# Kernel optimization log

Hardware: AMD Instinct MI355X
Metric: run time of the kernel (lower is better)

## Reference

```python
import jax, jax.numpy as jnp
import numpy as np

DIM = 1024
HEADS = 16
HEAD_DIM = DIM // HEADS


def setup_inputs() -> dict:
    key = jax.random.key(0)
    k_x, k_qkv, k_ow, k_ob = jax.random.split(key, 4)
    x = jax.random.normal(k_x, (2, 2048, DIM), dtype=jnp.float32)
    # nn.Linear(dim, 3*dim, bias=False): weight shape [3*dim, dim], y = x @ W.T
    w_qkv = jax.random.normal(k_qkv, (3 * DIM, DIM), dtype=jnp.float32) * (DIM ** -0.5)
    # nn.Linear(dim, dim) with bias
    w_o = jax.random.normal(k_ow, (DIM, DIM), dtype=jnp.float32) * (DIM ** -0.5)
    b_o = jax.random.normal(k_ob, (DIM,), dtype=jnp.float32) * 0.02
    return {"x": x, "w_qkv": w_qkv, "w_o": w_o, "b_o": b_o}


def reference(x, w_qkv, w_o, b_o):
    b, n, _ = x.shape
    scale = DIM ** -0.5  # NOTE: source scales by full dim, not head dim
    # qkv projection: [b, n, 3*dim]
    qkv = jnp.einsum('bnd,ed->bne', x, w_qkv)
    # 'b n (qkv h d) -> qkv b h n d'
    qkv = qkv.reshape(b, n, 3, HEADS, HEAD_DIM)
    q = jnp.transpose(qkv[:, :, 0], (0, 2, 1, 3))  # [b, h, n, d]
    k = jnp.transpose(qkv[:, :, 1], (0, 2, 1, 3))
    v = jnp.transpose(qkv[:, :, 2], (0, 2, 1, 3))
    scores = jnp.einsum('bhqd,bhkd->bhqk', q, k) * scale  # [b, h, n, n]
    attn = jax.nn.softmax(scores, axis=-1)
    out = jnp.einsum('bhqk,bhkd->bhqd', attn, v)  # [b, h, n, d]
    out = jnp.transpose(out, (0, 2, 1, 3)).reshape(b, n, DIM)  # 'b h n d -> b n (h d)'
    out = jnp.einsum('bnd,ed->bne', out, w_o) + b_o
    return out
```

## Files before the change

### kernel.cpp

```cpp
#include <hip/hip_runtime.h>
#include <stdint.h>


#define DIM 1024
#define SEQ 2048
#define BATCH 2
#define ROWS 4096
#define RSTRIDE 3072

typedef __bf16 bf16_t;
typedef bf16_t bf16x4 __attribute__((ext_vector_type(4)));
typedef bf16_t bf16x8 __attribute__((ext_vector_type(8)));
typedef float f32x4 __attribute__((ext_vector_type(4)));

__device__ __forceinline__ ushort f2bf(float f) {
    uint32_t u;
    __builtin_memcpy(&u, &f, 4);
    uint32_t r = (u + 0x7fffu + ((u >> 16) & 1u)) >> 16;
    return (ushort)r;
}

__device__ __forceinline__ void store_out(ushort* p, float v) { *p = f2bf(v); }
__device__ __forceinline__ void store_out(float* p, float v) { *p = v; }

__device__ __forceinline__ void gl_lds16(const void* g, void* l) {
    __builtin_amdgcn_global_load_lds(
        (const __attribute__((address_space(1))) void*)g,
        (__attribute__((address_space(3))) void*)l, 16, 0, 0);
}

__global__ __launch_bounds__(256) void cvt_kernel(
    const float* __restrict__ src, ushort* __restrict__ dst) {
    int i = (blockIdx.x * 256 + threadIdx.x) * 8;
    float4 a = *(const float4*)(src + i);
    float4 b = *(const float4*)(src + i + 4);
    uint4 u;
    u.x = (uint)f2bf(a.x) | ((uint)f2bf(a.y) << 16);
    u.y = (uint)f2bf(a.z) | ((uint)f2bf(a.w) << 16);
    u.z = (uint)f2bf(b.x) | ((uint)f2bf(b.y) << 16);
    u.w = (uint)f2bf(b.z) | ((uint)f2bf(b.w) << 16);
    *(uint4*)(dst + i) = u;
}

template <typename OutT>
__global__ __launch_bounds__(256) void gemm_bt_kernel(
    const ushort* __restrict__ A, const ushort* __restrict__ B,
    const float* __restrict__ bias, OutT* __restrict__ C,
    int M, int N, int K) {
    __shared__ __align__(16) ushort sA[128 * 64];
    __shared__ __align__(16) ushort sB[128 * 64];

    const int tid = threadIdx.x;
    const int lane = tid & 63, w = tid >> 6;
    const int quad = lane >> 4, l15 = lane & 15;
    const int wm = (w >> 1) * 64, wn = (w & 1) * 64;
    const int bm = blockIdx.y, bn = blockIdx.x;

    f32x4 acc[4][4];
#pragma unroll
    for (int i = 0; i < 4; i++)
#pragma unroll
        for (int j = 0; j < 4; j++) acc[i][j] = (f32x4){0.f, 0.f, 0.f, 0.f};

    const ushort* Abase = A + (size_t)(bm * 128) * K;
    const ushort* Bbase = B + (size_t)(bn * 128) * K;
    const int rd = lane >> 3, c8 = lane & 7;
    const int sw = l15 & 7;

    for (int kk = 0; kk < K; kk += 64) {
        __syncthreads();
#pragma unroll
        for (int t = 0; t < 4; t++) {
            int row = w * 32 + t * 8;
            gl_lds16(Abase + (size_t)(row + rd) * K + kk + ((c8 ^ rd) * 8),
                     sA + row * 64);
            gl_lds16(Bbase + (size_t)(row + rd) * K + kk + ((c8 ^ rd) * 8),
                     sB + row * 64);
        }
        __syncthreads();

#pragma unroll
        for (int kh = 0; kh < 2; kh++) {
            bf16x8 af[4], bfr[4];
#pragma unroll
            for (int i = 0; i < 4; i++)
                af[i] = *(const bf16x8*)((const bf16_t*)sA +
                        (wm + i * 16 + l15) * 64 + (((kh * 4 + quad) ^ sw) * 8));
#pragma unroll
            for (int j = 0; j < 4; j++)
                bfr[j] = *(const bf16x8*)((const bf16_t*)sB +
                        (wn + j * 16 + l15) * 64 + (((kh * 4 + quad) ^ sw) * 8));
#pragma unroll
            for (int i = 0; i < 4; i++)
#pragma unroll
                for (int j = 0; j < 4; j++)
                    acc[i][j] = __builtin_amdgcn_mfma_f32_16x16x32_bf16(
                        af[i], bfr[j], acc[i][j], 0, 0, 0);
        }
    }

#pragma unroll
    for (int i = 0; i < 4; i++)
#pragma unroll
        for (int j = 0; j < 4; j++) {
            int col = bn * 128 + wn + j * 16 + l15;
            float bv = bias ? bias[col] : 0.f;
#pragma unroll
            for (int r = 0; r < 4; r++) {
                int row = bm * 128 + wm + i * 16 + quad * 4 + r;
                store_out(&C[(size_t)row * N + col], acc[i][j][r] + bv);
            }
        }
}

__global__ __launch_bounds__(512) void flash_attn_kernel(
    const ushort* __restrict__ qkv, ushort* __restrict__ out) {
    __shared__ __align__(16) ushort sK[128 * 72];
    __shared__ __align__(16) ushort sVt[64 * 136];
    __shared__ __align__(16) ushort sP[128 * 68];

    const int tid = threadIdx.x;
    const int lane = tid & 63, w = tid >> 6;
    const int quad = lane >> 4, l15 = lane & 15;
    const int bh = blockIdx.y, b = bh >> 4, h = bh & 15;
    const int q0 = blockIdx.x * 128;
    const ushort* qkvb = qkv + (size_t)b * SEQ * RSTRIDE + h * 64;

    const ushort* qrow = qkvb + (size_t)(q0 + w * 16 + l15) * RSTRIDE;
    const bf16x8 aq0 = *(const bf16x8*)(qrow + quad * 8);
    const bf16x8 aq1 = *(const bf16x8*)(qrow + 32 + quad * 8);

    const int krow = tid >> 3, kc8 = tid & 7;
    const int vrp = tid & 63, vc = tid >> 6;

    uint4 kreg0, kreg1, va, vb;
    {
        const ushort* kp0 = qkvb + (size_t)krow * RSTRIDE + DIM + kc8 * 8;
        kreg0 = *(const uint4*)kp0;
        kreg1 = *(const uint4*)(kp0 + (size_t)64 * RSTRIDE);
        const ushort* v0 = qkvb + (size_t)(2 * vrp) * RSTRIDE + 2 * DIM + vc * 8;
        va = *(const uint4*)v0;
        vb = *(const uint4*)(v0 + RSTRIDE);
    }

    f32x4 l_acc = (f32x4){0.f, 0.f, 0.f, 0.f};
    f32x4 o[4];
#pragma unroll
    for (int j = 0; j < 4; j++) o[j] = (f32x4){0.f, 0.f, 0.f, 0.f};

    bf16x8 vones;
#pragma unroll
    for (int e = 0; e < 8; e++) vones[e] = (bf16_t)1.0f;

    const float c_exp = 0.04508422f;

    uint* vt32 = (uint*)sVt;
    for (int kb = 0; kb < SEQ; kb += 128) {
        *(uint4*)(sK + krow * 72 + kc8 * 8) = kreg0;
        *(uint4*)(sK + (krow + 64) * 72 + kc8 * 8) = kreg1;
        {
            int base = (vc * 8) * 68 + vrp;
            vt32[base + 0 * 68] = (va.x & 0xffffu) | (vb.x << 16);
            vt32[base + 1 * 68] = (va.x >> 16) | (vb.x & 0xffff0000u);
            vt32[base + 2 * 68] = (va.y & 0xffffu) | (vb.y << 16);
            vt32[base + 3 * 68] = (va.y >> 16) | (vb.y & 0xffff0000u);
            vt32[base + 4 * 68] = (va.z & 0xffffu) | (vb.z << 16);
            vt32[base + 5 * 68] = (va.z >> 16) | (vb.z & 0xffff0000u);
            vt32[base + 6 * 68] = (va.w & 0xffffu) | (vb.w << 16);
            vt32[base + 7 * 68] = (va.w >> 16) | (vb.w & 0xffff0000u);
        }
        __syncthreads();

        int nkb = (kb + 128 < SEQ) ? kb + 128 : kb;
        {
            const ushort* kp0 = qkvb + (size_t)(nkb + krow) * RSTRIDE + DIM + kc8 * 8;
            kreg0 = *(const uint4*)kp0;
            kreg1 = *(const uint4*)(kp0 + (size_t)64 * RSTRIDE);
            const ushort* v0 =
                qkvb + (size_t)(nkb + 2 * vrp) * RSTRIDE + 2 * DIM + vc * 8;
            va = *(const uint4*)v0;
            vb = *(const uint4*)(v0 + RSTRIDE);
        }

        f32x4 s[8];
#pragma unroll
        for (int j = 0; j < 8; j++) {
            const ushort* kp = sK + (j * 16 + l15) * 72;
            bf16x8 bk0 = *(const bf16x8*)(kp + quad * 8);
            bf16x8 bk1 = *(const bf16x8*)(kp + 32 + quad * 8);
            f32x4 z = (f32x4){0.f, 0.f, 0.f, 0.f};
            z = __builtin_amdgcn_mfma_f32_16x16x32_bf16(aq0, bk0, z, 0, 0, 0);
            z = __builtin_amdgcn_mfma_f32_16x16x32_bf16(aq1, bk1, z, 0, 0, 0);
            s[j] = z;
        }

#pragma unroll
        for (int h2 = 0; h2 < 2; h2++) {
#pragma unroll
            for (int j = 0; j < 4; j++)
#pragma unroll
                for (int r = 0; r < 4; r++) {
                    float p = __builtin_amdgcn_exp2f(s[h2 * 4 + j][r] * c_exp);
                    sP[(w * 16 + quad * 4 + r) * 68 + j * 16 + l15] = f2bf(p);
                }
            const bf16_t* pp = (const bf16_t*)sP + (w * 16 + l15) * 68;
            bf16x4 pl0 = *(const bf16x4*)(pp + quad * 8);
            bf16x4 ph0 = *(const bf16x4*)(pp + quad * 8 + 4);
            bf16x4 pl1 = *(const bf16x4*)(pp + 32 + quad * 8);
            bf16x4 ph1 = *(const bf16x4*)(pp + 32 + quad * 8 + 4);
            bf16x8 pa0 = __builtin_shufflevector(pl0, ph0, 0, 1, 2, 3, 4, 5, 6, 7);
            bf16x8 pa1 = __builtin_shufflevector(pl1, ph1, 0, 1, 2, 3, 4, 5, 6, 7);
            l_acc = __builtin_amdgcn_mfma_f32_16x16x32_bf16(pa0, vones, l_acc, 0, 0, 0);
            l_acc = __builtin_amdgcn_mfma_f32_16x16x32_bf16(pa1, vones, l_acc, 0, 0, 0);
#pragma unroll
            for (int jd = 0; jd < 4; jd++) {
                const bf16_t* vp =
                    (const bf16_t*)sVt + (jd * 16 + l15) * 136 + h2 * 64;
                bf16x8 bv0 = *(const bf16x8*)(vp + quad * 8);
                bf16x8 bv1 = *(const bf16x8*)(vp + 32 + quad * 8);
                o[jd] = __builtin_amdgcn_mfma_f32_16x16x32_bf16(pa0, bv0, o[jd], 0, 0, 0);
                o[jd] = __builtin_amdgcn_mfma_f32_16x16x32_bf16(pa1, bv1, o[jd], 0, 0, 0);
            }
        }
        __syncthreads();
    }

#pragma unroll
    for (int r = 0; r < 4; r++) {
        float inv = 1.f / l_acc[r];
        int qrow_i = q0 + w * 16 + quad * 4 + r;
#pragma unroll
        for (int j = 0; j < 4; j++) {
            out[(size_t)(b * SEQ + qrow_i) * DIM + h * 64 + j * 16 + l15] =
                f2bf(o[j][r] * inv);
        }
    }
}

extern "C" void kernel_launch(void* const* d_in, const int* in_sizes, int n_in,
                              void* d_out, int out_size, void* d_ws, size_t ws_size,
                              hipStream_t stream) {
    const float* x = (const float*)d_in[0];
    const float* w_qkv = (const float*)d_in[1];
    const float* w_o = (const float*)d_in[2];
    const float* b_o = (const float*)d_in[3];
    float* out = (float*)d_out;

    ushort* qkv = (ushort*)d_ws;
    ushort* attn = qkv + (size_t)ROWS * 3 * DIM;
    ushort* xb = attn + (size_t)ROWS * DIM;
    ushort* wqkvb = xb + (size_t)ROWS * DIM;
    ushort* wob = wqkvb + (size_t)3 * DIM * DIM;

    dim3 blk(256);
    cvt_kernel<<<ROWS * DIM / 2048, blk, 0, stream>>>(x, xb);
    cvt_kernel<<<3 * DIM * DIM / 2048, blk, 0, stream>>>(w_qkv, wqkvb);
    cvt_kernel<<<DIM * DIM / 2048, blk, 0, stream>>>(w_o, wob);

    gemm_bt_kernel<ushort><<<dim3(3 * DIM / 128, ROWS / 128), blk, 0, stream>>>(
        xb, wqkvb, nullptr, qkv, ROWS, 3 * DIM, DIM);
    flash_attn_kernel<<<dim3(SEQ / 128, BATCH * 16), dim3(512), 0, stream>>>(qkv, attn);
    gemm_bt_kernel<float><<<dim3(DIM / 128, ROWS / 128), blk, 0, stream>>>(
        attn, wob, b_o, out, ROWS, DIM, DIM);
}
```

Baseline: 219.4 us.

## Replace padded LDS tiles with XOR-swizzled layouts and raise MFMA wave priority

Removes row padding from the K, V-transposed and P shared-memory tiles and uses XOR swizzles on 16-byte chunks instead, so bank conflicts are avoided without the wasted LDS. P reads become single 128-bit loads rather than two 64-bit loads plus a shuffle. The bf16 conversion of P now uses a native cast instead of the manual rounding helper. MFMA calls are wrapped in s_setprio to favor matrix issue across waves, which risks perturbing scheduling and needs the swizzle indexing to be exactly consistent between writers and readers.

```diff
diff --git a/kernel.cpp b/kernel.cpp
--- a/kernel.cpp
+++ b/kernel.cpp
@@ -115,13 +115,14 @@
 
 __global__ __launch_bounds__(512) void flash_attn_kernel(
     const ushort* __restrict__ qkv, ushort* __restrict__ out) {
-    __shared__ __align__(16) ushort sK[128 * 72];
-    __shared__ __align__(16) ushort sVt[64 * 136];
-    __shared__ __align__(16) ushort sP[128 * 68];
+    __shared__ __align__(16) ushort sK[128 * 64];
+    __shared__ __align__(16) ushort sVt[64 * 128];
+    __shared__ __align__(16) ushort sP[128 * 64];
 
     const int tid = threadIdx.x;
     const int lane = tid & 63, w = tid >> 6;
     const int quad = lane >> 4, l15 = lane & 15;
+    const int sw = l15 & 7;
     const int bh = blockIdx.y, b = bh >> 4, h = bh & 15;
     const int q0 = blockIdx.x * 128;
     const ushort* qkvb = qkv + (size_t)b * SEQ * RSTRIDE + h * 64;
@@ -131,7 +132,9 @@
     const bf16x8 aq1 = *(const bf16x8*)(qrow + 32 + quad * 8);
 
     const int krow = tid >> 3, kc8 = tid & 7;
+    const int kdst = krow * 64 + ((kc8 ^ (krow & 7)) * 8);
     const int vrp = tid & 63, vc = tid >> 6;
+    const int vch = vrp >> 2, vlo = vrp & 3;
 
     uint4 kreg0, kreg1, va, vb;
     {
@@ -155,19 +158,20 @@
     const float c_exp = 0.04508422f;
 
     uint* vt32 = (uint*)sVt;
+    bf16_t* sPb = (bf16_t*)sP;
     for (int kb = 0; kb < SEQ; kb += 128) {
-        *(uint4*)(sK + krow * 72 + kc8 * 8) = kreg0;
-        *(uint4*)(sK + (krow + 64) * 72 + kc8 * 8) = kreg1;
+        *(uint4*)(sK + kdst) = kreg0;
+        *(uint4*)(sK + 64 * 64 + kdst) = kreg1;
         {
-            int base = (vc * 8) * 68 + vrp;
-            vt32[base + 0 * 68] = (va.x & 0xffffu) | (vb.x << 16);
-            vt32[base + 1 * 68] = (va.x >> 16) | (vb.x & 0xffff0000u);
-            vt32[base + 2 * 68] = (va.y & 0xffffu) | (vb.y << 16);
-            vt32[base + 3 * 68] = (va.y >> 16) | (vb.y & 0xffff0000u);
-            vt32[base + 4 * 68] = (va.z & 0xffffu) | (vb.z << 16);
-            vt32[base + 5 * 68] = (va.z >> 16) | (vb.z & 0xffff0000u);
-            vt32[base + 6 * 68] = (va.w & 0xffffu) | (vb.w << 16);
-            vt32[base + 7 * 68] = (va.w >> 16) | (vb.w & 0xffff0000u);
+            int base = (vc * 8) * 64 + vlo;
+            vt32[base + 0 * 64 + ((vch ^ 0) << 2)] = (va.x & 0xffffu) | (vb.x << 16);
+            vt32[base + 1 * 64 + ((vch ^ 1) << 2)] = (va.x >> 16) | (vb.x & 0xffff0000u);
+            vt32[base + 2 * 64 + ((vch ^ 2) << 2)] = (va.y & 0xffffu) | (vb.y << 16);
+            vt32[base + 3 * 64 + ((vch ^ 3) << 2)] = (va.y >> 16) | (vb.y & 0xffff0000u);
+            vt32[base + 4 * 64 + ((vch ^ 4) << 2)] = (va.z & 0xffffu) | (vb.z << 16);
+            vt32[base + 5 * 64 + ((vch ^ 5) << 2)] = (va.z >> 16) | (vb.z & 0xffff0000u);
+            vt32[base + 6 * 64 + ((vch ^ 6) << 2)] = (va.w & 0xffffu) | (vb.w << 16);
+            vt32[base + 7 * 64 + ((vch ^ 7) << 2)] = (va.w >> 16) | (vb.w & 0xffff0000u);
         }
         __syncthreads();
 
@@ -185,12 +189,14 @@
         f32x4 s[8];
 #pragma unroll
         for (int j = 0; j < 8; j++) {
-            const ushort* kp = sK + (j * 16 + l15) * 72;
-            bf16x8 bk0 = *(const bf16x8*)(kp + quad * 8);
-            bf16x8 bk1 = *(const bf16x8*)(kp + 32 + quad * 8);
+            const ushort* kp = sK + (j * 16 + l15) * 64;
+            bf16x8 bk0 = *(const bf16x8*)(kp + ((quad ^ sw) * 8));
+            bf16x8 bk1 = *(const bf16x8*)(kp + (((4 | quad) ^ sw) * 8));
             f32x4 z = (f32x4){0.f, 0.f, 0.f, 0.f};
+            __builtin_amdgcn_s_setprio(1);
             z = __builtin_amdgcn_mfma_f32_16x16x32_bf16(aq0, bk0, z, 0, 0, 0);
             z = __builtin_amdgcn_mfma_f32_16x16x32_bf16(aq1, bk1, z, 0, 0, 0);
+            __builtin_amdgcn_s_setprio(0);
             s[j] = z;
         }
 
@@ -201,25 +207,28 @@
 #pragma unroll
                 for (int r = 0; r < 4; r++) {
                     float p = __builtin_amdgcn_exp2f(s[h2 * 4 + j][r] * c_exp);
-                    sP[(w * 16 + quad * 4 + r) * 68 + j * 16 + l15] = f2bf(p);
+                    int row = w * 16 + quad * 4 + r;
+                    int ch = j * 2 + (l15 >> 3);
+                    sPb[row * 64 +
+                        (((ch ^ ((quad * 4 + r) & 7)) << 3) | (l15 & 7))] =
+                        (bf16_t)p;
                 }
-            const bf16_t* pp = (const bf16_t*)sP + (w * 16 + l15) * 68;
-            bf16x4 pl0 = *(const bf16x4*)(pp + quad * 8);
-            bf16x4 ph0 = *(const bf16x4*)(pp + quad * 8 + 4);
-            bf16x4 pl1 = *(const bf16x4*)(pp + 32 + quad * 8);
-            bf16x4 ph1 = *(const bf16x4*)(pp + 32 + quad * 8 + 4);
-            bf16x8 pa0 = __builtin_shufflevector(pl0, ph0, 0, 1, 2, 3, 4, 5, 6, 7);
-            bf16x8 pa1 = __builtin_shufflevector(pl1, ph1, 0, 1, 2, 3, 4, 5, 6, 7);
+            const bf16_t* pp = sPb + (w * 16 + l15) * 64;
+            bf16x8 pa0 = *(const bf16x8*)(pp + ((quad ^ sw) * 8));
+            bf16x8 pa1 = *(const bf16x8*)(pp + (((4 | quad) ^ sw) * 8));
+            __builtin_amdgcn_s_setprio(1);
             l_acc = __builtin_amdgcn_mfma_f32_16x16x32_bf16(pa0, vones, l_acc, 0, 0, 0);
             l_acc = __builtin_amdgcn_mfma_f32_16x16x32_bf16(pa1, vones, l_acc, 0, 0, 0);
+            __builtin_amdgcn_s_setprio(0);
 #pragma unroll
             for (int jd = 0; jd < 4; jd++) {
-                const bf16_t* vp =
-                    (const bf16_t*)sVt + (jd * 16 + l15) * 136 + h2 * 64;
-                bf16x8 bv0 = *(const bf16x8*)(vp + quad * 8);
-                bf16x8 bv1 = *(const bf16x8*)(vp + 32 + quad * 8);
+                const bf16_t* vp = (const bf16_t*)sVt + (jd * 16 + l15) * 128;
+                bf16x8 bv0 = *(const bf16x8*)(vp + (((h2 * 8 + quad) ^ sw) * 8));
+                bf16x8 bv1 = *(const bf16x8*)(vp + (((h2 * 8 + 4 + quad) ^ sw) * 8));
+                __builtin_amdgcn_s_setprio(1);
                 o[jd] = __builtin_amdgcn_mfma_f32_16x16x32_bf16(pa0, bv0, o[jd], 0, 0, 0);
                 o[jd] = __builtin_amdgcn_mfma_f32_16x16x32_bf16(pa1, bv1, o[jd], 0, 0, 0);
+                __builtin_amdgcn_s_setprio(0);
             }
         }
         __syncthreads();
```

Result: faster. 200.2 us (-8.8%).
